# Performance work log

Hardware: AMD Instinct MI355X
Metric: run time of the kernel (lower is better)

The kernel has to match this reference:

```python
import jax, jax.numpy as jnp
import numpy as np

FP, ENC, H, OUT, STEPS = 4860, 512, 512, 42, 128


def _lin(k, fan_in, fan_out, scale=0.02):
    kw, kb = jax.random.split(k)
    W = jax.random.normal(kw, (fan_out, fan_in), jnp.float32) * scale
    b = jax.random.normal(kb, (fan_out,), jnp.float32) * scale
    return W, b


def setup_inputs() -> dict:
    key = jax.random.key(0)
    ks = jax.random.split(key, 12)
    x = jax.random.normal(ks[0], (2048, FP), jnp.float32)
    y = jax.random.normal(ks[1], (2048, STEPS, OUT), jnp.float32)
    eps = jax.random.normal(ks[2], (2048, ENC), jnp.float32)
    We1, be1 = _lin(ks[3], FP, 2048)
    We2, be2 = _lin(ks[4], 2048, 1024)
    We3, be3 = _lin(ks[5], 1024, 512)
    We41, be41 = _lin(ks[6], 512, ENC)
    Wih, bih = _lin(ks[7], ENC, 3 * H)    # GRU input weights [3H, ENC]
    Whh, bhh = _lin(ks[8], H, 3 * H)      # GRU hidden weights [3H, H]
    Wf1, bf1 = _lin(ks[9], H, OUT)        # EncoderDecoder.fc1
    Wf2, bf2 = _lin(ks[10], OUT, H)       # EncoderDecoder.fc2
    return dict(x=x, y=y, eps=eps,
                We1=We1, be1=be1, We2=We2, be2=be2, We3=We3, be3=be3,
                We41=We41, be41=be41,
                Wih=Wih, bih=bih, Whh=Whh, bhh=bhh,
                Wf1=Wf1, bf1=bf1, Wf2=Wf2, bf2=bf2,
                teacher_forcing=0)


def _forward(x, eps, We1, be1, We2, be2, We3, be3, We41, be41,
             Wih, bih, Whh, bhh, Wf1, bf1, Wf2, bf2):
    # VAE encoder (note: source uses fc41 for BOTH mu and logvar)
    h1 = jax.nn.relu(x @ We1.T + be1)
    h2 = jax.nn.relu(h1 @ We2.T + be2)
    h3 = jax.nn.relu(h2 @ We3.T + be3)
    mu = h3 @ We41.T + be41
    logvar = mu
    encoded = eps * jnp.exp(0.5 * logvar) + mu  # reparameterize, [B, ENC]

    B = x.shape[0]
    h0 = jnp.zeros((B, H), x.dtype)

    def step(carry, _):
        h, xt = carry                      # h: [B,H], xt: [B,ENC]
        gi = xt @ Wih.T + bih              # [B,3H]
        gh = h @ Whh.T + bhh               # [B,3H]
        r = jax.nn.sigmoid(gi[:, :H] + gh[:, :H])
        z = jax.nn.sigmoid(gi[:, H:2 * H] + gh[:, H:2 * H])
        n = jnp.tanh(gi[:, 2 * H:] + r * gh[:, 2 * H:])
        h_new = (1.0 - z) * n + z * h
        out = jax.nn.relu(h_new @ Wf1.T + bf1)   # [B,42]
        x_new = jax.nn.relu(out @ Wf2.T + bf2)   # [B,H] (no teacher forcing)
        return (h_new, x_new), out

    (_, _), outs = jax.lax.scan(step, (h0, encoded), None, length=STEPS)
    return jnp.transpose(outs, (1, 0, 2))  # [B, 128, 42]


def reference(x, y, eps, We1, be1, We2, be2, We3, be3, We41, be41,
              Wih, bih, Whh, bhh, Wf1, bf1, Wf2, bf2, teacher_forcing):
    # teacher_forcing=0 (False path); y unused in that branch.
    return _forward(x, eps, We1, be1, We2, be2, We3, be3, We41, be41,
                    Wih, bih, Whh, bhh, Wf1, bf1, Wf2, bf2)
```

## Files before the change

kernel.cpp:

```cpp
#include <hip/hip_runtime.h>
#include <hip/hip_bf16.h>
#include <cstdint>
#include <cstddef>

#define DEVI __device__ __forceinline__

typedef __attribute__((ext_vector_type(8))) short bf16x8;
typedef __attribute__((ext_vector_type(4))) float f32x4;
typedef unsigned short u16;
typedef unsigned int u32;
typedef unsigned long long u64;

DEVI u16 f2bf(float f) {
    u32 i = __builtin_bit_cast(u32, f);
    u32 r = (i + 0x7FFFu + ((i >> 16) & 1u)) >> 16;
    return (u16)r;
}
DEVI float sigmoidf_(float x) { return 1.0f / (1.0f + __expf(-x)); }
DEVI float tanhf_(float x) { return 2.0f / (1.0f + __expf(-2.0f * x)) - 1.0f; }
DEVI float reluf_(float x) { return x > 0.f ? x : 0.f; }

typedef const __attribute__((address_space(1))) void* gptr_t;
typedef __attribute__((address_space(3))) void* lptr_t;

DEVI void gload16(const void* g, void* l) {
    __builtin_amdgcn_global_load_lds((gptr_t)g, (lptr_t)l, 16, 0, 0);
}

__global__ void fill_const(float* __restrict__ p, int n, float v) {
    int i = blockIdx.x * 256 + threadIdx.x;
    if (i < n) p[i] = v;
}

__global__ void prep_all(const float* __restrict__ x, const float* __restrict__ We1,
                         const float* __restrict__ We2, const float* __restrict__ We3,
                         const float* __restrict__ We41, const float* __restrict__ Wih,
                         const float* __restrict__ Whh, const float* __restrict__ Wf1,
                         const float* __restrict__ Wf2, u16* __restrict__ xb,
                         u16* __restrict__ We1b, u16* __restrict__ We2b,
                         u16* __restrict__ We3b, u16* __restrict__ We41b,
                         u16* __restrict__ WB, u16* __restrict__ Wf1p,
                         u16* __restrict__ Wf2p) {
    const long long T0 = 9961472, T1 = 19922944, T2 = 22020096, T3 = 22544384,
                    T4 = 22806528, T5 = 23592960, T6 = 24379392, T7 = 24403968,
                    T8 = 24436736;
    for (long long i = (long long)blockIdx.x * 256 + threadIdx.x; i < T8;
         i += (long long)gridDim.x * 256) {
        if (i < T1) {
            long long j = (i < T0) ? i : i - T0;
            int r = (int)(j / 4864);
            int c = (int)(j - (long long)r * 4864);
            const float* s = (i < T0) ? x : We1;
            u16* d = (i < T0) ? xb : We1b;
            d[j] = (c < 4860) ? f2bf(s[(size_t)r * 4860 + c]) : (u16)0;
        } else if (i < T2) {
            int j = (int)(i - T1);
            We2b[j] = f2bf(We2[j]);
        } else if (i < T3) {
            int j = (int)(i - T2);
            We3b[j] = f2bf(We3[j]);
        } else if (i < T4) {
            int j = (int)(i - T3);
            We41b[j] = f2bf(We41[j]);
        } else if (i < T5) {
            int j = (int)(i - T4);
            int g = j >> 9, k = j & 511;
            WB[(size_t)g * 1024 + k] = f2bf(Wih[j]);
        } else if (i < T6) {
            int j = (int)(i - T5);
            int g = j >> 9, k = j & 511;
            WB[(size_t)g * 1024 + 512 + k] = f2bf(Whh[j]);
        } else if (i < T7) {
            int j = (int)(i - T6);
            int r = j >> 9;
            Wf1p[j] = (r < 42) ? f2bf(Wf1[j]) : (u16)0;
        } else {
            int j = (int)(i - T7);
            int c = j >> 6, k = j & 63;
            Wf2p[j] = (k < 42) ? f2bf(Wf2[(size_t)c * 42 + k]) : (u16)0;
        }
    }
}

template <int EPI>
__global__ __launch_bounds__(256) void gemm_bt(
    const u16* __restrict__ A, int lda, const u16* __restrict__ B, int ldb,
    const float* __restrict__ bias, u16* __restrict__ C, int ldc, int ktiles,
    const float* __restrict__ eps) {
    __shared__ u16 As[128 * 64];
    __shared__ u16 Bs[128 * 64];
    const int tid = threadIdx.x;
    const int lane = tid & 63;
    const int wave = tid >> 6;
    const int m0 = blockIdx.y * 128;
    const int n0 = blockIdx.x * 128;
    const int l15 = lane & 15, lg = lane >> 4;
    const int wm = (wave >> 1) * 64, wn = (wave & 1) * 64;

    f32x4 acc[4][4];
#pragma unroll
    for (int r = 0; r < 4; r++)
#pragma unroll
        for (int c = 0; c < 4; c++) acc[r][c] = (f32x4){0.f, 0.f, 0.f, 0.f};

    for (int t = 0; t < ktiles; ++t) {
        const int k0 = t * 64;
#pragma unroll
        for (int q = 0; q < 4; ++q) {
            int chunk = q * 4 + wave;
            int o = chunk * 1024 + lane * 16;
            int row = o >> 7;
            int cb = o & 127;
            gload16((const char*)(A + (size_t)(m0 + row) * lda + k0) + cb,
                    (char*)As + chunk * 1024);
            gload16((const char*)(B + (size_t)(n0 + row) * ldb + k0) + cb,
                    (char*)Bs + chunk * 1024);
        }
        __syncthreads();
#pragma unroll
        for (int kf = 0; kf < 2; ++kf) {
            bf16x8 a[4], b[4];
#pragma unroll
            for (int r = 0; r < 4; r++)
                a[r] = *(const bf16x8*)&As[(wm + 16 * r + l15) * 64 + kf * 32 + lg * 8];
#pragma unroll
            for (int c = 0; c < 4; c++)
                b[c] = *(const bf16x8*)&Bs[(wn + 16 * c + l15) * 64 + kf * 32 + lg * 8];
#pragma unroll
            for (int r = 0; r < 4; r++)
#pragma unroll
                for (int c = 0; c < 4; c++)
                    acc[r][c] = __builtin_amdgcn_mfma_f32_16x16x32_bf16(
                        a[r], b[c], acc[r][c], 0, 0, 0);
        }
        __syncthreads();
    }
#pragma unroll
    for (int r = 0; r < 4; r++) {
#pragma unroll
        for (int c = 0; c < 4; c++) {
            int col = n0 + wn + 16 * c + l15;
            float bv = bias[col];
#pragma unroll
            for (int i = 0; i < 4; i++) {
                int row = m0 + wm + 16 * r + lg * 4 + i;
                float v = acc[r][c][i] + bv;
                if (EPI == 0) {
                    v = v > 0.f ? v : 0.f;
                    C[(size_t)row * ldc + col] = f2bf(v);
                } else {
                    float e = eps[(size_t)row * 512 + col];
                    float enc = e * __expf(0.5f * v) + v;
                    C[(size_t)row * ldc + col] = f2bf(enc);
                }
            }
        }
    }
}

template <int MODE>
__global__ __launch_bounds__(1024, 1) void gru_step(
    const u16* __restrict__ xt0, const u16* __restrict__ hbR,
    const float* __restrict__ hfR, u16* __restrict__ hbW,
    float* __restrict__ hfW, const u16* __restrict__ WB,
    const float* __restrict__ bih, const float* __restrict__ bhh,
    const u16* __restrict__ Wf1p, const float* __restrict__ bf1,
    const u16* __restrict__ Wf2p, const float* __restrict__ bf2,
    float* __restrict__ outp, int sidx) {
    __shared__ __align__(16) u16 xtL[64 * 512];
    __shared__ __align__(16) u16 Bst[2][192 * 64];
    __shared__ __align__(16) u16 oL[64 * 64];
    const int tid = threadIdx.x, lane = tid & 63, wave = tid >> 6;
    const int wr = wave >> 2, wu = wave & 3;
    const int l15 = lane & 15, lg = lane >> 4;
    const int bid = blockIdx.x;
    const int sb = (MODE == 2) ? 0 : (bid & 7);
    const int rb = (MODE == 2) ? bid : (bid >> 3);
    const int S = sb * 64, m0 = rb * 64;
    const int sw = (l15 & 7) << 4;

    if (MODE == 0) {
#pragma unroll
        for (int k2 = 0; k2 < 4; ++k2) {
            int j = tid + k2 * 1024;
            int row = j >> 6, slot = j & 63;
            gload16((const char*)(xt0 + (size_t)(m0 + row) * 512) + (slot ^ (row & 7)) * 16,
                    (char*)xtL + j * 16);
        }
    }

    if (MODE >= 1) {
        if (MODE == 1) {
            ((u64*)oL)[tid] = 0ull;
            __syncthreads();
        }
        if (wu < 3) {
            f32x4 oa = (f32x4){0.f, 0.f, 0.f, 0.f};
            const u16* ha = hbR + (size_t)(m0 + 16 * wr + l15) * 512 + lg * 8;
            const u16* wb1 = Wf1p + (size_t)(16 * wu + l15) * 512 + lg * 8;
#pragma unroll
            for (int kf = 0; kf < 16; ++kf) {
                bf16x8 a = *(const bf16x8*)(ha + kf * 32);
                bf16x8 b = *(const bf16x8*)(wb1 + kf * 32);
                oa = __builtin_amdgcn_mfma_f32_16x16x32_bf16(a, b, oa, 0, 0, 0);
            }
            int col = 16 * wu + l15;
            float bv = (col < 42) ? bf1[col] : 0.f;
#pragma unroll
            for (int i = 0; i < 4; ++i) {
                int row = 16 * wr + lg * 4 + i;
                float v = reluf_(oa[i] + bv);
                if (col >= 42) v = 0.f;
                if (MODE == 1) {
                    int cb = col * 2;
                    *(u16*)((char*)oL + row * 128 +
                            (((cb & ~15) ^ ((row & 7) << 4)) | (cb & 15))) = f2bf(v);
                }
                if (sb == 0 && col < 42)
                    outp[(size_t)(m0 + row) * 5376 + (size_t)sidx * 42 + col] = v;
            }
        }
    }

    if (MODE == 1) {
        __syncthreads();
        bf16x8 a2[2];
#pragma unroll
        for (int kf = 0; kf < 2; ++kf) {
            int row = 16 * wr + l15;
            a2[kf] = *(const bf16x8*)((char*)oL + row * 128 +
                                      ((kf * 64 + lg * 16) ^ ((row & 7) << 4)));
        }
#pragma unroll
        for (int ci = 0; ci < 8; ++ci) {
            int col = 128 * wu + 16 * ci + l15;
            const u16* wb2 = Wf2p + (size_t)col * 64 + lg * 8;
            f32x4 xa = (f32x4){0.f, 0.f, 0.f, 0.f};
            xa = __builtin_amdgcn_mfma_f32_16x16x32_bf16(a2[0], *(const bf16x8*)wb2, xa, 0, 0, 0);
            xa = __builtin_amdgcn_mfma_f32_16x16x32_bf16(a2[1], *(const bf16x8*)(wb2 + 32), xa, 0, 0, 0);
            float bv = bf2[col];
            int cb = col * 2;
#pragma unroll
            for (int i = 0; i < 4; ++i) {
                int row = 16 * wr + lg * 4 + i;
                float v = reluf_(xa[i] + bv);
                *(u16*)((char*)xtL + row * 1024 +
                        (((cb & ~15) ^ ((row & 7) << 4)) | (cb & 15))) = f2bf(v);
            }
        }
    }

    if (MODE <= 1) {
        __syncthreads();

        auto stageB = [&](int buf, int t) {
            {
                int j = tid;
                int row = j >> 3, slot = j & 7;
                int gate = row >> 6, unit = row & 63;
                gload16(WB + (size_t)(gate * 512 + S + unit) * 1024 + t * 64 +
                            (slot ^ (row & 7)) * 8,
                        (char*)Bst + buf * 24576 + j * 16);
            }
            if (tid < 512) {
                int j = tid + 1024;
                int row = j >> 3, slot = j & 7;
                int gate = row >> 6, unit = row & 63;
                gload16(WB + (size_t)(gate * 512 + S + unit) * 1024 + t * 64 +
                            (slot ^ (row & 7)) * 8,
                        (char*)Bst + buf * 24576 + j * 16);
            }
        };
        f32x4 ar = (f32x4){0.f, 0.f, 0.f, 0.f};
        f32x4 az = ar, agi = ar, agh = ar;
        const int arow = 16 * wr + l15;
        const u16* hrow = hbR + (size_t)(m0 + arow) * 512 + lg * 8;
        bf16x8 hc0, hc1, hp0, hp1;

        stageB(0, 0);
        for (int t = 0; t < 16; ++t) {
            if (t >= 7 && t < 15) {
                const u16* hs = hrow + (t - 7) * 64;
                hp0 = *(const bf16x8*)hs;
                hp1 = *(const bf16x8*)(hs + 32);
            }
            if (t < 15) stageB((t + 1) & 1, t + 1);
            __builtin_amdgcn_sched_barrier(0);
            if (t == 15) {
                asm volatile("s_waitcnt vmcnt(0)");
            } else if (t >= 7) {
                if (wave < 8) asm volatile("s_waitcnt vmcnt(4)");
                else          asm volatile("s_waitcnt vmcnt(3)");
            } else {
                if (wave < 8) asm volatile("s_waitcnt vmcnt(2)");
                else          asm volatile("s_waitcnt vmcnt(1)");
            }
            __builtin_amdgcn_sched_barrier(0);
            __builtin_amdgcn_s_barrier();
            __builtin_amdgcn_sched_barrier(0);

            bf16x8 a[2];
            if (t < 8) {
#pragma unroll
                for (int kf = 0; kf < 2; ++kf)
                    a[kf] = *(const bf16x8*)((char*)xtL + arow * 1024 +
                                             ((t * 128 + kf * 64 + lg * 16) ^ sw));
            } else {
                a[0] = hc0;
                a[1] = hc1;
            }
            const char* bb = (const char*)Bst + (t & 1) * 24576;
            int rb0 = 16 * wu + l15;
            int swb = (rb0 & 7) << 4;
#pragma unroll
            for (int kf = 0; kf < 2; ++kf) {
                int kb = kf * 64 + lg * 16;
                bf16x8 br = *(const bf16x8*)(bb + (size_t)rb0 * 128 + (kb ^ swb));
                bf16x8 bz = *(const bf16x8*)(bb + (size_t)(64 + rb0) * 128 + (kb ^ swb));
                bf16x8 bn = *(const bf16x8*)(bb + (size_t)(128 + rb0) * 128 + (kb ^ swb));
                ar = __builtin_amdgcn_mfma_f32_16x16x32_bf16(a[kf], br, ar, 0, 0, 0);
                az = __builtin_amdgcn_mfma_f32_16x16x32_bf16(a[kf], bz, az, 0, 0, 0);
                if (t < 8)
                    agi = __builtin_amdgcn_mfma_f32_16x16x32_bf16(a[kf], bn, agi, 0, 0, 0);
                else
                    agh = __builtin_amdgcn_mfma_f32_16x16x32_bf16(a[kf], bn, agh, 0, 0, 0);
            }
            hc0 = hp0;
            hc1 = hp1;
            __builtin_amdgcn_sched_barrier(0);
            __builtin_amdgcn_s_barrier();
        }
        int hu = S + 16 * wu + l15;
        float br_ = bih[hu] + bhh[hu];
        float bz_ = bih[512 + hu] + bhh[512 + hu];
        float bgi = bih[1024 + hu];
        float bgh = bhh[1024 + hu];
#pragma unroll
        for (int i = 0; i < 4; ++i) {
            int row = m0 + 16 * wr + lg * 4 + i;
            float rv = sigmoidf_(ar[i] + br_);
            float zv = sigmoidf_(az[i] + bz_);
            float nv = tanhf_(agi[i] + bgi + rv * (agh[i] + bgh));
            float hold = hfR[(size_t)row * 512 + hu];
            float hn = (1.f - zv) * nv + zv * hold;
            hfW[(size_t)row * 512 + hu] = hn;
            hbW[(size_t)row * 512 + hu] = f2bf(hn);
        }
    }
}

extern "C" void kernel_launch(void* const* d_in, const int* in_sizes, int n_in,
                              void* d_out, int out_size, void* d_ws,
                              size_t ws_size, hipStream_t stream) {
    (void)in_sizes; (void)n_in; (void)out_size;
    const float* x = (const float*)d_in[0];
    const float* eps = (const float*)d_in[2];
    const float* We1 = (const float*)d_in[3];
    const float* be1 = (const float*)d_in[4];
    const float* We2 = (const float*)d_in[5];
    const float* be2 = (const float*)d_in[6];
    const float* We3 = (const float*)d_in[7];
    const float* be3 = (const float*)d_in[8];
    const float* We41 = (const float*)d_in[9];
    const float* be41 = (const float*)d_in[10];
    const float* Wih = (const float*)d_in[11];
    const float* bih = (const float*)d_in[12];
    const float* Whh = (const float*)d_in[13];
    const float* bhh = (const float*)d_in[14];
    const float* Wf1 = (const float*)d_in[15];
    const float* bf1 = (const float*)d_in[16];
    const float* Wf2 = (const float*)d_in[17];
    const float* bf2 = (const float*)d_in[18];
    float* out = (float*)d_out;

    char* ws = (char*)d_ws;
    size_t off = 0;
    auto alloc = [&](size_t bytes) -> char* {
        char* p = ws + off;
        off += (bytes + 255) & ~(size_t)255;
        return p;
    };
    u16* xb = (u16*)alloc(2048ull * 4864 * 2);
    u16* We1b = (u16*)alloc(2048ull * 4864 * 2);
    u16* We2b = (u16*)alloc(1024ull * 2048 * 2);
    u16* We3b = (u16*)alloc(512ull * 1024 * 2);
    u16* We41b = (u16*)alloc(512ull * 512 * 2);
    u16* WB = (u16*)alloc(1536ull * 1024 * 2);
    u16* h1b = (u16*)alloc(2048ull * 2048 * 2);
    u16* h2b = (u16*)alloc(2048ull * 1024 * 2);
    u16* h3b = (u16*)alloc(2048ull * 512 * 2);
    u16* encb = (u16*)alloc(2048ull * 512 * 2);
    u16* hb0 = (u16*)alloc(2048ull * 512 * 2);
    u16* hb1 = (u16*)alloc(2048ull * 512 * 2);
    float* hf0 = (float*)alloc(2048ull * 512 * 4);
    float* hf1 = (float*)alloc(2048ull * 512 * 4);
    u16* Wf1p = (u16*)alloc(48ull * 512 * 2);
    u16* Wf2p = (u16*)alloc(512ull * 64 * 2);
    if (off > ws_size) {
        fill_const<<<(11010048 + 255) / 256, 256, 0, stream>>>(out, 11010048, 54321.0f);
        return;
    }
    u16* hb[2] = {hb0, hb1};
    float* hfl[2] = {hf0, hf1};

    prep_all<<<8192, 256, 0, stream>>>(x, We1, We2, We3, We41, Wih, Whh, Wf1, Wf2,
                                       xb, We1b, We2b, We3b, We41b, WB, Wf1p, Wf2p);
    hipMemsetAsync(hb0, 0, 2048ull * 512 * 2, stream);
    hipMemsetAsync(hf0, 0, 2048ull * 512 * 4, stream);

    gemm_bt<0><<<dim3(16, 16), 256, 0, stream>>>(xb, 4864, We1b, 4864, be1, h1b, 2048, 76, nullptr);
    gemm_bt<0><<<dim3(8, 16), 256, 0, stream>>>(h1b, 2048, We2b, 2048, be2, h2b, 1024, 32, nullptr);
    gemm_bt<0><<<dim3(4, 16), 256, 0, stream>>>(h2b, 1024, We3b, 1024, be3, h3b, 512, 16, nullptr);
    gemm_bt<1><<<dim3(4, 16), 256, 0, stream>>>(h3b, 512, We41b, 512, be41, encb, 512, 8, eps);

    gru_step<0><<<256, 1024, 0, stream>>>(encb, hb0, hf0, hb1, hf1, WB, bih,
                                          bhh, Wf1p, bf1, Wf2p, bf2, out, 0);
    for (int i = 1; i < 128; ++i) {
        int p = i & 1;
        gru_step<1><<<256, 1024, 0, stream>>>(nullptr, hb[p], hfl[p],
                                              hb[p ^ 1], hfl[p ^ 1], WB, bih,
                                              bhh, Wf1p, bf1, Wf2p, bf2, out,
                                              i - 1);
    }
    gru_step<2><<<32, 1024, 0, stream>>>(nullptr, hb0, hf0, nullptr, nullptr,
                                         WB, bih, bhh, Wf1p, bf1, Wf2p, bf2,
                                         out, 127);
}
```

Before: 4.844 ms.

## Replace per-step GRU kernel launches with a persistent cooperative kernel using grid sync

The 129 separate gru_step launches are replaced by one cooperative persistent kernel that loops over all 128 timesteps. Steps are separated by grid.sync, and the hidden state is exchanged through global memory using cache-bypassing loads and stores. Each thread keeps its fp32 hidden state in registers instead of round-tripping an fp32 buffer, and weights are streamed in smaller 32-wide k tiles. The aim is to remove per-launch overhead and the fp32 state traffic. The cost is a grid-wide barrier every step, and the old launch path is kept as a fallback if the cooperative launch fails.

After: 16.24 ms. 235% more time.

```diff
diff --git a/kernel.cpp b/kernel.cpp
--- a/kernel.cpp
+++ b/kernel.cpp
@@ -1,7 +1,10 @@
 #include <hip/hip_runtime.h>
 #include <hip/hip_bf16.h>
+#include <hip/hip_cooperative_groups.h>
 #include <cstdint>
 #include <cstddef>
+
+namespace cg = cooperative_groups;
 
 #define DEVI __device__ __forceinline__
 
@@ -25,6 +28,15 @@
 
 DEVI void gload16(const void* g, void* l) {
     __builtin_amdgcn_global_load_lds((gptr_t)g, (lptr_t)l, 16, 0, 0);
+}
+
+DEVI f32x4 glc16(const void* p) {
+    f32x4 r;
+    asm volatile("global_load_dwordx4 %0, %1, off sc0 sc1" : "=v"(r) : "v"(p));
+    return r;
+}
+DEVI void stg_sc1_u16(void* p, u32 v) {
+    asm volatile("global_store_short %0, %1, off sc0 sc1" ::"v"(p), "v"(v));
 }
 
 __global__ void fill_const(float* __restrict__ p, int n, float v) {
@@ -158,6 +170,183 @@
     }
 }
 
+__global__ __launch_bounds__(1024, 1) void gru_persist(
+    const u16* __restrict__ encb, u16* __restrict__ hb0, u16* __restrict__ hb1,
+    const u16* __restrict__ WB, const float* __restrict__ bih,
+    const float* __restrict__ bhh, const u16* __restrict__ Wf1p,
+    const float* __restrict__ bf1, const u16* __restrict__ Wf2p,
+    const float* __restrict__ bf2, float* __restrict__ outp) {
+    __shared__ __align__(16) u16 hT[64 * 512];
+    __shared__ __align__(16) u16 xtL[64 * 512];
+    __shared__ __align__(16) u16 Bst[2][192 * 32];
+    u16* oL = (u16*)Bst;
+    cg::grid_group grid = cg::this_grid();
+    const int tid = threadIdx.x, lane = tid & 63, wave = tid >> 6;
+    const int wr = wave >> 2, wu = wave & 3;
+    const int l15 = lane & 15, lg = lane >> 4;
+    const int bid = blockIdx.x;
+    const int sb = bid & 7, rb = bid >> 3;
+    const int S = sb * 64, m0 = rb * 64;
+    const int sw = (l15 & 7) << 4;
+
+#pragma unroll
+    for (int k2 = 0; k2 < 4; ++k2) {
+        int j = tid + k2 * 1024;
+        int row = j >> 6, slot = j & 63;
+        gload16((const char*)(encb + (size_t)(m0 + row) * 512) + (slot ^ (row & 7)) * 16,
+                (char*)xtL + j * 16);
+    }
+    {
+        u64* hz = (u64*)hT;
+#pragma unroll
+        for (int k2 = 0; k2 < 8; ++k2) hz[tid + k2 * 1024] = 0ull;
+    }
+    f32x4 hreg = (f32x4){0.f, 0.f, 0.f, 0.f};
+    const int hu = S + 16 * wu + l15;
+    const float br_ = bih[hu] + bhh[hu];
+    const float bz_ = bih[512 + hu] + bhh[512 + hu];
+    const float bgi = bih[1024 + hu];
+    const float bgh = bhh[1024 + hu];
+
+    for (int it = 0; it <= 128; ++it) {
+        if (it > 0) {
+            const u16* hbR = (it & 1) ? hb1 : hb0;
+            f32x4 v[4];
+#pragma unroll
+            for (int k2 = 0; k2 < 4; ++k2) {
+                int j = tid + k2 * 1024;
+                int row = j >> 6, slot = j & 63;
+                v[k2] = glc16((const char*)(hbR + (size_t)(m0 + row) * 512) +
+                              (slot ^ (row & 7)) * 16);
+            }
+            asm volatile("s_waitcnt vmcnt(0)" ::: "memory");
+            __builtin_amdgcn_sched_barrier(0);
+#pragma unroll
+            for (int k2 = 0; k2 < 4; ++k2) {
+                int j = tid + k2 * 1024;
+                *(f32x4*)((char*)hT + j * 16) = v[k2];
+            }
+            __syncthreads();
+
+            if (wu < 3) {
+                f32x4 oa = (f32x4){0.f, 0.f, 0.f, 0.f};
+                const u16* wb1 = Wf1p + (size_t)(16 * wu + l15) * 512 + lg * 8;
+                const int arow = 16 * wr + l15;
+#pragma unroll
+                for (int kf = 0; kf < 16; ++kf) {
+                    bf16x8 a = *(const bf16x8*)((char*)hT + arow * 1024 +
+                                                ((kf * 64 + lg * 16) ^ sw));
+                    oa = __builtin_amdgcn_mfma_f32_16x16x32_bf16(
+                        a, *(const bf16x8*)(wb1 + kf * 32), oa, 0, 0, 0);
+                }
+                int col = 16 * wu + l15;
+                float bv = (col < 42) ? bf1[col] : 0.f;
+#pragma unroll
+                for (int i = 0; i < 4; ++i) {
+                    int row = 16 * wr + lg * 4 + i;
+                    float v2 = reluf_(oa[i] + bv);
+                    if (col >= 42) v2 = 0.f;
+                    int cb = col * 2;
+                    *(u16*)((char*)oL + row * 128 +
+                            (((cb & ~15) ^ ((row & 7) << 4)) | (cb & 15))) = f2bf(v2);
+                    if (sb == 0 && col < 42)
+                        outp[(size_t)(m0 + row) * 5376 + (size_t)(it - 1) * 42 + col] = v2;
+                }
+            }
+            if (it == 128) break;
+            __syncthreads();
+
+            bf16x8 a2[2];
+#pragma unroll
+            for (int kf = 0; kf < 2; ++kf) {
+                int row = 16 * wr + l15;
+                a2[kf] = *(const bf16x8*)((char*)oL + row * 128 +
+                                          ((kf * 64 + lg * 16) ^ ((row & 7) << 4)));
+            }
+#pragma unroll
+            for (int ci = 0; ci < 8; ++ci) {
+                int col = 128 * wu + 16 * ci + l15;
+                const u16* wb2 = Wf2p + (size_t)col * 64 + lg * 8;
+                f32x4 xa = (f32x4){0.f, 0.f, 0.f, 0.f};
+                xa = __builtin_amdgcn_mfma_f32_16x16x32_bf16(a2[0], *(const bf16x8*)wb2, xa, 0, 0, 0);
+                xa = __builtin_amdgcn_mfma_f32_16x16x32_bf16(a2[1], *(const bf16x8*)(wb2 + 32), xa, 0, 0, 0);
+                float bv = bf2[col];
+                int cb = col * 2;
+#pragma unroll
+                for (int i = 0; i < 4; ++i) {
+                    int row = 16 * wr + lg * 4 + i;
+                    float v2 = reluf_(xa[i] + bv);
+                    *(u16*)((char*)xtL + row * 1024 +
+                            (((cb & ~15) ^ ((row & 7) << 4)) | (cb & 15))) = f2bf(v2);
+                }
+            }
+        }
+        __syncthreads();
+
+        auto stageB = [&](int buf, int t) {
+            if (tid < 768) {
+                int j = tid;
+                int row = j >> 2, slot = j & 3;
+                int gate = row >> 6, unit = row & 63;
+                gload16(WB + (size_t)(gate * 512 + S + unit) * 1024 + t * 32 +
+                            (slot ^ (row & 3)) * 8,
+                        (char*)Bst + buf * 12288 + j * 16);
+            }
+        };
+        f32x4 ar = (f32x4){0.f, 0.f, 0.f, 0.f};
+        f32x4 az = ar, agi = ar, agh = ar;
+        const int arow = 16 * wr + l15;
+        const int brow = 16 * wu + l15;
+
+        stageB(0, 0);
+        for (int t = 0; t < 32; ++t) {
+            if (t < 31) stageB((t + 1) & 1, t + 1);
+            __builtin_amdgcn_sched_barrier(0);
+            if (tid < 768 && t < 31) {
+                asm volatile("s_waitcnt vmcnt(1)");
+            } else {
+                asm volatile("s_waitcnt vmcnt(0)");
+            }
+            __builtin_amdgcn_sched_barrier(0);
+            __builtin_amdgcn_s_barrier();
+            __builtin_amdgcn_sched_barrier(0);
+
+            bf16x8 a;
+            if (t < 16)
+                a = *(const bf16x8*)((char*)xtL + arow * 1024 + ((t * 64 + lg * 16) ^ sw));
+            else
+                a = *(const bf16x8*)((char*)hT + arow * 1024 + (((t - 16) * 64 + lg * 16) ^ sw));
+            const char* bb = (const char*)Bst + (t & 1) * 12288;
+            bf16x8 br = *(const bf16x8*)(bb + (size_t)brow * 64 + ((lg * 16) ^ ((brow & 3) << 4)));
+            bf16x8 bz = *(const bf16x8*)(bb + (size_t)(64 + brow) * 64 + ((lg * 16) ^ ((brow & 3) << 4)));
+            bf16x8 bn = *(const bf16x8*)(bb + (size_t)(128 + brow) * 64 + ((lg * 16) ^ ((brow & 3) << 4)));
+            ar = __builtin_amdgcn_mfma_f32_16x16x32_bf16(a, br, ar, 0, 0, 0);
+            az = __builtin_amdgcn_mfma_f32_16x16x32_bf16(a, bz, az, 0, 0, 0);
+            if (t < 16)
+                agi = __builtin_amdgcn_mfma_f32_16x16x32_bf16(a, bn, agi, 0, 0, 0);
+            else
+                agh = __builtin_amdgcn_mfma_f32_16x16x32_bf16(a, bn, agh, 0, 0, 0);
+            __builtin_amdgcn_sched_barrier(0);
+            __builtin_amdgcn_s_barrier();
+        }
+
+        u16* hbW = (it & 1) ? hb0 : hb1;
+#pragma unroll
+        for (int i = 0; i < 4; ++i) {
+            int row = m0 + 16 * wr + lg * 4 + i;
+            float rv = sigmoidf_(ar[i] + br_);
+            float zv = sigmoidf_(az[i] + bz_);
+            float nv = tanhf_(agi[i] + bgi + rv * (agh[i] + bgh));
+            float hn = (1.f - zv) * nv + zv * hreg[i];
+            hreg[i] = hn;
+            stg_sc1_u16(hbW + (size_t)row * 512 + hu, (u32)f2bf(hn));
+        }
+        asm volatile("s_waitcnt vmcnt(0)" ::: "memory");
+        __threadfence();
+        grid.sync();
+    }
+}
+
 template <int MODE>
 __global__ __launch_bounds__(1024, 1) void gru_step(
     const u16* __restrict__ xt0, const u16* __restrict__ hbR,
@@ -188,7 +377,6 @@
                     (char*)xtL + j * 16);
         }
     }
-
     if (MODE >= 1) {
         if (MODE == 1) {
             ((u64*)oL)[tid] = 0ull;
@@ -221,7 +409,6 @@
             }
         }
     }
-
     if (MODE == 1) {
         __syncthreads();
         bf16x8 a2[2];
@@ -249,10 +436,8 @@
             }
         }
     }
-
     if (MODE <= 1) {
         __syncthreads();
-
         auto stageB = [&](int buf, int t) {
             {
                 int j = tid;
@@ -276,7 +461,6 @@
         const int arow = 16 * wr + l15;
         const u16* hrow = hbR + (size_t)(m0 + arow) * 512 + lg * 8;
         bf16x8 hc0, hc1, hp0, hp1;
-
         stageB(0, 0);
         for (int t = 0; t < 16; ++t) {
             if (t >= 7 && t < 15) {
@@ -298,7 +482,6 @@
             __builtin_amdgcn_sched_barrier(0);
             __builtin_amdgcn_s_barrier();
             __builtin_amdgcn_sched_barrier(0);
-
             bf16x8 a[2];
             if (t < 8) {
 #pragma unroll
@@ -400,19 +583,29 @@
         fill_const<<<(11010048 + 255) / 256, 256, 0, stream>>>(out, 11010048, 54321.0f);
         return;
     }
-    u16* hb[2] = {hb0, hb1};
-    float* hfl[2] = {hf0, hf1};
 
     prep_all<<<8192, 256, 0, stream>>>(x, We1, We2, We3, We41, Wih, Whh, Wf1, Wf2,
                                        xb, We1b, We2b, We3b, We41b, WB, Wf1p, Wf2p);
-    hipMemsetAsync(hb0, 0, 2048ull * 512 * 2, stream);
-    hipMemsetAsync(hf0, 0, 2048ull * 512 * 4, stream);
 
     gemm_bt<0><<<dim3(16, 16), 256, 0, stream>>>(xb, 4864, We1b, 4864, be1, h1b, 2048, 76, nullptr);
     gemm_bt<0><<<dim3(8, 16), 256, 0, stream>>>(h1b, 2048, We2b, 2048, be2, h2b, 1024, 32, nullptr);
     gemm_bt<0><<<dim3(4, 16), 256, 0, stream>>>(h2b, 1024, We3b, 1024, be3, h3b, 512, 16, nullptr);
     gemm_bt<1><<<dim3(4, 16), 256, 0, stream>>>(h3b, 512, We41b, 512, be41, encb, 512, 8, eps);
 
+    {
+        const u16* encb_a = encb;
+        void* kargs[] = {(void*)&encb_a, &hb0, &hb1, &WB, (void*)&bih, (void*)&bhh,
+                         &Wf1p, (void*)&bf1, &Wf2p, (void*)&bf2, &out};
+        hipError_t e = hipLaunchCooperativeKernel((const void*)gru_persist,
+                                                  dim3(256), dim3(1024), kargs, 0, stream);
+        if (e == hipSuccess) return;
+        (void)hipGetLastError();
+    }
+
+    hipMemsetAsync(hb0, 0, 2048ull * 512 * 2, stream);
+    hipMemsetAsync(hf0, 0, 2048ull * 512 * 4, stream);
+    u16* hb[2] = {hb0, hb1};
+    float* hfl[2] = {hf0, hf1};
     gru_step<0><<<256, 1024, 0, stream>>>(encb, hb0, hf0, hb1, hf1, WB, bih,
                                           bhh, Wf1p, bf1, Wf2p, bf2, out, 0);
     for (int i = 1; i < 128; ++i) {
```

## Deepen GRU weight staging to triple buffer and split fc1 accumulator chain

Applied to the files above, without the earlier changes.

The GRU step's weight-tile staging goes from double to triple buffering, prefetching two K-tiles ahead. The h-fragment register prefetch gets one more stage, and the vmcnt waits are retuned to match. The fc1 MFMA reduction is split into four independent accumulators to shorten the dependency chain. Together these aim to hide more global-load latency in the per-step kernel, at the cost of an extra 24KB of LDS and more registers, which could affect occupancy at 1024 threads.

Measured after the change: 4.741 ms (median of 2 runs). 1.02x faster.

```diff
diff --git a/kernel.cpp b/kernel.cpp
--- a/kernel.cpp
+++ b/kernel.cpp
@@ -168,7 +168,7 @@
     const u16* __restrict__ Wf2p, const float* __restrict__ bf2,
     float* __restrict__ outp, int sidx) {
     __shared__ __align__(16) u16 xtL[64 * 512];
-    __shared__ __align__(16) u16 Bst[2][192 * 64];
+    __shared__ __align__(16) u16 Bst[3][192 * 64];
     __shared__ __align__(16) u16 oL[64 * 64];
     const int tid = threadIdx.x, lane = tid & 63, wave = tid >> 6;
     const int wr = wave >> 2, wu = wave & 3;
@@ -195,15 +195,22 @@
             __syncthreads();
         }
         if (wu < 3) {
-            f32x4 oa = (f32x4){0.f, 0.f, 0.f, 0.f};
+            f32x4 oa0 = (f32x4){0.f, 0.f, 0.f, 0.f};
+            f32x4 oa1 = oa0, oa2 = oa0, oa3 = oa0;
             const u16* ha = hbR + (size_t)(m0 + 16 * wr + l15) * 512 + lg * 8;
             const u16* wb1 = Wf1p + (size_t)(16 * wu + l15) * 512 + lg * 8;
 #pragma unroll
-            for (int kf = 0; kf < 16; ++kf) {
-                bf16x8 a = *(const bf16x8*)(ha + kf * 32);
-                bf16x8 b = *(const bf16x8*)(wb1 + kf * 32);
-                oa = __builtin_amdgcn_mfma_f32_16x16x32_bf16(a, b, oa, 0, 0, 0);
-            }
+            for (int kf = 0; kf < 4; ++kf) {
+                oa0 = __builtin_amdgcn_mfma_f32_16x16x32_bf16(
+                    *(const bf16x8*)(ha + kf * 32), *(const bf16x8*)(wb1 + kf * 32), oa0, 0, 0, 0);
+                oa1 = __builtin_amdgcn_mfma_f32_16x16x32_bf16(
+                    *(const bf16x8*)(ha + (kf + 4) * 32), *(const bf16x8*)(wb1 + (kf + 4) * 32), oa1, 0, 0, 0);
+                oa2 = __builtin_amdgcn_mfma_f32_16x16x32_bf16(
+                    *(const bf16x8*)(ha + (kf + 8) * 32), *(const bf16x8*)(wb1 + (kf + 8) * 32), oa2, 0, 0, 0);
+                oa3 = __builtin_amdgcn_mfma_f32_16x16x32_bf16(
+                    *(const bf16x8*)(ha + (kf + 12) * 32), *(const bf16x8*)(wb1 + (kf + 12) * 32), oa3, 0, 0, 0);
+            }
+            f32x4 oa = (oa0 + oa1) + (oa2 + oa3);
             int col = 16 * wu + l15;
             float bv = (col < 42) ? bf1[col] : 0.f;
 #pragma unroll
@@ -275,25 +282,32 @@
         f32x4 az = ar, agi = ar, agh = ar;
         const int arow = 16 * wr + l15;
         const u16* hrow = hbR + (size_t)(m0 + arow) * 512 + lg * 8;
-        bf16x8 hc0, hc1, hp0, hp1;
+        bf16x8 hc0, hc1, hp1a, hp1b, hp2a, hp2b;
 
         stageB(0, 0);
+        stageB(1, 1);
         for (int t = 0; t < 16; ++t) {
-            if (t >= 7 && t < 15) {
-                const u16* hs = hrow + (t - 7) * 64;
-                hp0 = *(const bf16x8*)hs;
-                hp1 = *(const bf16x8*)(hs + 32);
-            }
-            if (t < 15) stageB((t + 1) & 1, t + 1);
+            if (t >= 6 && t < 14) {
+                const u16* hs = hrow + (t - 6) * 64;
+                hp2a = *(const bf16x8*)hs;
+                hp2b = *(const bf16x8*)(hs + 32);
+            }
+            if (t < 14) stageB((t + 2) % 3, t + 2);
             __builtin_amdgcn_sched_barrier(0);
-            if (t == 15) {
-                asm volatile("s_waitcnt vmcnt(0)");
-            } else if (t >= 7) {
+            if (t < 6) {
+                if (wave < 8) asm volatile("s_waitcnt vmcnt(4)");
+                else          asm volatile("s_waitcnt vmcnt(2)");
+            } else if (t == 6) {
+                if (wave < 8) asm volatile("s_waitcnt vmcnt(6)");
+                else          asm volatile("s_waitcnt vmcnt(4)");
+            } else if (t < 14) {
+                if (wave < 8) asm volatile("s_waitcnt vmcnt(8)");
+                else          asm volatile("s_waitcnt vmcnt(6)");
+            } else if (t == 14) {
                 if (wave < 8) asm volatile("s_waitcnt vmcnt(4)");
                 else          asm volatile("s_waitcnt vmcnt(3)");
             } else {
-                if (wave < 8) asm volatile("s_waitcnt vmcnt(2)");
-                else          asm volatile("s_waitcnt vmcnt(1)");
+                asm volatile("s_waitcnt vmcnt(0)");
             }
             __builtin_amdgcn_sched_barrier(0);
             __builtin_amdgcn_s_barrier();
@@ -309,7 +323,7 @@
                 a[0] = hc0;
                 a[1] = hc1;
             }
-            const char* bb = (const char*)Bst + (t & 1) * 24576;
+            const char* bb = (const char*)Bst + (t % 3) * 24576;
             int rb0 = 16 * wu + l15;
             int swb = (rb0 & 7) << 4;
 #pragma unroll
@@ -325,8 +339,10 @@
                 else
                     agh = __builtin_amdgcn_mfma_f32_16x16x32_bf16(a[kf], bn, agh, 0, 0, 0);
             }
-            hc0 = hp0;
-            hc1 = hp1;
+            hc0 = hp1a;
+            hc1 = hp1b;
+            hp1a = hp2a;
+            hp1b = hp2b;
             __builtin_amdgcn_sched_barrier(0);
             __builtin_amdgcn_s_barrier();
         }
```
